# Optimization experiments

Hardware: AMD Instinct MI355X
Metric: run time of the kernel (lower is better)

Reference implementation:

```python
import jax, jax.numpy as jnp
import numpy as np

# Geometry: 256x256 image, 16x16 superpixel grid (cell=16), K=256, C=20 features, B=4.
B, H, W, C, KG = 4, 256, 256, 20, 16
K = KG * KG
CELL = H // KG
BIG_DIST = 1e4  # additive distance for non-neighbor superpixels


def setup_inputs() -> dict:
    key = jax.random.key(0)
    kf, = jax.random.split(key, 1)
    # initial hard pixel->superpixel grid assignment (get_spixel_init)
    gy = jnp.arange(H) // CELL
    gx = jnp.arange(W) // CELL
    spixel_init = (gy[:, None] * KG + gx[None, :]).reshape(-1).astype(jnp.int32)  # [N]
    # 9-neighborhood validity mask (compute_neighbor_spix_idx)
    ky = jnp.arange(K) // KG
    kx = jnp.arange(K) % KG
    pgy = spixel_init // KG
    pgx = spixel_init % KG
    valid = ((jnp.abs(pgy[:, None] - ky[None, :]) <= 1)
             & (jnp.abs(pgx[:, None] - kx[None, :]) <= 1)).astype(jnp.float32)  # [N, K]
    adjust = (1.0 - valid) * BIG_DIST  # [N, K]
    features = jax.random.normal(kf, (B, H * W, C), dtype=jnp.float32)  # CNN output, flattened
    return {
        "features": features,
        "valid_spixel": valid,
        "adjust_dist": adjust,
        "spixel_init": spixel_init,
        "iter_EM": 10,
    }


def _e_step(mean, features, valid_spixel, adjust_dist):
    # squared distances via ||f||^2 - 2 f.m + ||m||^2 (bmm form)
    feat_sq = jnp.sum(features * features, axis=-1)        # [B, N]
    mean_sq = jnp.sum(mean * mean, axis=-1)                # [B, K]
    dot = jnp.einsum('bnc,bkc->bnk', features, mean)       # [B, N, K]
    dist_sq = feat_sq[:, :, None] - 2.0 * dot + mean_sq[:, None, :]
    dist_sq = dist_sq * valid_spixel[None] + adjust_dist[None]
    # std = 1/sqrt(2) => 2*std^2 = 1, so softmax argument is -dist_sq
    return jax.nn.softmax(-dist_sq, axis=2)                # [B, N, K]


def _m_step(features, posteriors):
    # L1-normalize posteriors over the pixel axis (dim=1), then weighted mean
    col = jnp.maximum(jnp.sum(posteriors, axis=1, keepdims=True), 1e-12)
    post_norm = posteriors / col
    return jnp.einsum('bnk,bnc->bkc', post_norm, features)  # [B, K, C]


def reference(features, valid_spixel, adjust_dist, spixel_init, iter_EM):
    # compute_init_spixel_feat: mean of features within each initial superpixel (detached in torch)
    n = features.shape[1]
    sums = jax.vmap(lambda f: jax.ops.segment_sum(f, spixel_init, num_segments=K))(features)  # [B, K, C]
    counts = jax.ops.segment_sum(jnp.ones((n,), features.dtype), spixel_init, num_segments=K)  # [K]
    mean = jax.lax.stop_gradient(sums / jnp.maximum(counts, 1.0)[None, :, None])
    for _ in range(int(iter_EM) - 1):
        posteriors = _e_step(mean, features, valid_spixel, adjust_dist)
        mean = _m_step(features, posteriors)
    return _e_step(mean, features, valid_spixel, adjust_dist)
```

## Files before the change

### kernel.cpp

```cpp
#include <hip/hip_runtime.h>


#define NBATCH 4
#define WIMG   256
#define NC     20
#define NCS    21
#define NKG    16
#define NK     256
#define NPIX   65536
#define CELLSZ 16
#define LDST   260

__device__ __forceinline__ float dot4f(const float4 a, const float4 b) {
    return fmaf(a.x, b.x, fmaf(a.y, b.y, fmaf(a.z, b.z, a.w * b.w)));
}

__device__ __forceinline__ void load_feat(const float* __restrict__ feat, int b, int n, float f[NC]) {
    const float4* fp = (const float4*)(feat + ((size_t)b * NPIX + n) * NC);
    #pragma unroll
    for (int i = 0; i < 5; ++i) {
        float4 v = fp[i];
        f[4 * i + 0] = v.x; f[4 * i + 1] = v.y; f[4 * i + 2] = v.z; f[4 * i + 3] = v.w;
    }
}

__device__ __forceinline__ void e_step(const float* f, int b, int cy, int cx,
                                       const float* __restrict__ Sprev, float p[9]) {
    float a[9];
    float amax = -1e30f;
    #pragma unroll
    for (int dy = -1; dy <= 1; ++dy) {
        #pragma unroll
        for (int dx = -1; dx <= 1; ++dx) {
            int j = (dy + 1) * 3 + (dx + 1);
            int ky = cy + dy, kx = cx + dx;
            if (ky >= 0 && ky < NKG && kx >= 0 && kx < NKG) {
                const float* sp = Sprev + ((size_t)(b * NK + ky * NKG + kx)) * NCS;
                float dots = 0.f, ssq = 0.f;
                #pragma unroll
                for (int c = 0; c < NC; ++c) {
                    float sv = sp[c];
                    dots = fmaf(f[c], sv, dots);
                    ssq  = fmaf(sv, sv, ssq);
                }
                float col = fmaxf(sp[NC], 1e-12f);
                float r = 1.0f / col;
                a[j] = 2.0f * r * dots - (r * r) * ssq;
                amax = fmaxf(amax, a[j]);
            } else {
                a[j] = -1e30f;
            }
        }
    }
    float esum = 0.f;
    #pragma unroll
    for (int j = 0; j < 9; ++j) {
        float e = (a[j] > -1e29f) ? __expf(a[j] - amax) : 0.0f;
        p[j] = e;
        esum += e;
    }
    float inv = 1.0f / esum;
    #pragma unroll
    for (int j = 0; j < 9; ++j) p[j] *= inv;
}

__global__ __launch_bounds__(256, 4) void k_init(const float* __restrict__ feat,
                                                 float* __restrict__ S0,
                                                 float* __restrict__ S1) {
    __shared__ float fT[NC * LDST];
    int blk = blockIdx.x;
    int b = blk >> 8, k0 = blk & 255;
    int cy = k0 >> 4, cx = k0 & 15;
    int t = threadIdx.x;
    int ly = t >> 4, lx = t & 15;
    int n = (cy * CELLSZ + ly) * WIMG + cx * CELLSZ + lx;
    float f[NC];
    load_feat(feat, b, n, f);
    #pragma unroll
    for (int c = 0; c < NC; ++c) fT[c * LDST + t] = f[c];
    __syncthreads();
    if (t < NCS) {
        float s;
        if (t == NC) {
            s = 256.0f;
        } else {
            s = 0.f;
            const float4* row = (const float4*)&fT[t * LDST];
            #pragma unroll 4
            for (int i = 0; i < 64; ++i) { float4 v = row[i]; s += v.x + v.y + v.z + v.w; }
        }
        size_t off = ((size_t)(b * NK + k0)) * NCS + t;
        S0[off] = s;
        S1[off] = 0.0f;
    }
}

__global__ __launch_bounds__(256, 4) void k_em(const float* __restrict__ feat,
                                               const float* __restrict__ Sprev,
                                               float* __restrict__ Snext,
                                               float* __restrict__ Szero) {
    __shared__ float fT[NCS * LDST];
    __shared__ float pT[9 * LDST];
    __shared__ float part[21 * 8 * 9];
    int blk = blockIdx.x;
    int b = blk >> 8, k0 = blk & 255;
    int cy = k0 >> 4, cx = k0 & 15;
    int t = threadIdx.x;
    int ly = t >> 4, lx = t & 15;
    int n = (cy * CELLSZ + ly) * WIMG + cx * CELLSZ + lx;
    float f[NC];
    load_feat(feat, b, n, f);
    #pragma unroll
    for (int c = 0; c < NC; ++c) fT[c * LDST + t] = f[c];
    fT[NC * LDST + t] = 1.0f;
    float p[9];
    e_step(f, b, cy, cx, Sprev, p);
    #pragma unroll
    for (int j = 0; j < 9; ++j) pT[j * LDST + t] = p[j];
    __syncthreads();

    if (t < 168) {
        int tile = t >> 3, kid = t & 7;
        int j0 = (tile / 7) * 3, c0 = (tile % 7) * 3;
        float acc[3][3] = {};
        #pragma unroll
        for (int ch = 0; ch < 8; ++ch) {
            int nb = kid * 32 + (((ch + kid) & 7) << 2);
            float4 pv[3], fv[3];
            #pragma unroll
            for (int jj = 0; jj < 3; ++jj) pv[jj] = *(const float4*)&pT[(j0 + jj) * LDST + nb];
            #pragma unroll
            for (int cc = 0; cc < 3; ++cc) fv[cc] = *(const float4*)&fT[(c0 + cc) * LDST + nb];
            #pragma unroll
            for (int jj = 0; jj < 3; ++jj)
                #pragma unroll
                for (int cc = 0; cc < 3; ++cc)
                    acc[jj][cc] += dot4f(pv[jj], fv[cc]);
        }
        #pragma unroll
        for (int jj = 0; jj < 3; ++jj)
            #pragma unroll
            for (int cc = 0; cc < 3; ++cc)
                part[tile * 72 + kid * 9 + jj * 3 + cc] = acc[jj][cc];
    }
    __syncthreads();
    if (t < 189) {
        int j = t / 21, c = t % 21;
        int tile = (j / 3) * 7 + (c / 3);
        int elem = (j % 3) * 3 + (c % 3);
        float s = 0.f;
        #pragma unroll
        for (int kid = 0; kid < 8; ++kid) s += part[tile * 72 + kid * 9 + elem];
        int ky = cy + (j / 3) - 1, kx = cx + (j % 3) - 1;
        if (ky >= 0 && ky < NKG && kx >= 0 && kx < NKG)
            atomicAdd(&Snext[((size_t)(b * NK + ky * NKG + kx)) * NCS + c], s);
    }
    if (t < NCS) Szero[((size_t)(b * NK + k0)) * NCS + t] = 0.0f;
}

__global__ __launch_bounds__(256, 4) void k_final(const float* __restrict__ feat,
                                                  const float* __restrict__ Sprev,
                                                  float* __restrict__ out) {
    __shared__ float pT[9 * LDST];
    int blk = blockIdx.x;
    int b = blk >> 8, k0 = blk & 255;
    int cy = k0 >> 4, cx = k0 & 15;
    int t = threadIdx.x;
    int ly = t >> 4, lx = t & 15;
    int n = (cy * CELLSZ + ly) * WIMG + cx * CELLSZ + lx;
    float f[NC];
    load_feat(feat, b, n, f);
    float p[9];
    e_step(f, b, cy, cx, Sprev, p);
    #pragma unroll
    for (int j = 0; j < 9; ++j) pT[j * LDST + t] = p[j];
    __syncthreads();

    int wv = t >> 6, ln = t & 63;
    int j4[4];
    #pragma unroll
    for (int q = 0; q < 4; ++q) {
        int k = 4 * ln + q;
        int ky = k >> 4, kx = k & 15;
        int dy = ky - cy, dx = kx - cx;
        j4[q] = (dy >= -1 && dy <= 1 && dx >= -1 && dx <= 1) ? (dy + 1) * 3 + (dx + 1) : -1;
    }
    for (int i = 0; i < 64; ++i) {
        int pix = wv * 64 + i;
        int py = pix >> 4, px = pix & 15;
        int np = (cy * CELLSZ + py) * WIMG + cx * CELLSZ + px;
        float4 o;
        o.x = (j4[0] >= 0) ? pT[j4[0] * LDST + pix] : 0.0f;
        o.y = (j4[1] >= 0) ? pT[j4[1] * LDST + pix] : 0.0f;
        o.z = (j4[2] >= 0) ? pT[j4[2] * LDST + pix] : 0.0f;
        o.w = (j4[3] >= 0) ? pT[j4[3] * LDST + pix] : 0.0f;
        size_t rowoff = ((size_t)(b * NPIX + np)) * (size_t)NK;
        *(float4*)(out + rowoff + 4 * ln) = o;
    }
}

extern "C" void kernel_launch(void* const* d_in, const int* in_sizes, int n_in,
                              void* d_out, int out_size, void* d_ws, size_t ws_size,
                              hipStream_t stream) {
    (void)in_sizes; (void)n_in; (void)out_size; (void)ws_size;
    const float* feat = (const float*)d_in[0];
    float* out = (float*)d_out;
    const size_t SB = (size_t)NBATCH * NK * NCS;
    float* bufs[3] = { (float*)d_ws, (float*)d_ws + SB, (float*)d_ws + 2 * SB };

    dim3 grid(NBATCH * NK), block(256);
    k_init<<<grid, block, 0, stream>>>(feat, bufs[0], bufs[1]);
    for (int i = 1; i <= 9; ++i) {
        k_em<<<grid, block, 0, stream>>>(feat, bufs[(i - 1) % 3], bufs[i % 3], bufs[(i + 1) % 3]);
    }
    k_final<<<grid, block, 0, stream>>>(feat, bufs[0], out);
}
```

Baseline: 545.4 us.

## Fuse init, EM iterations and final step into one cooperative persistent kernel

Replaces the eleven separate kernel launches with a single cooperative kernel that keeps each block's pixel features in registers and shared memory across all EM iterations, separating iterations with grid-wide syncs. This removes launch gaps and repeated feature loads from global memory. It depends on all 1024 blocks being co-resident; if the cooperative launch fails it falls back to the original multi-kernel path. Grid syncs add their own latency per iteration.

New measurement: 1.810 ms. 3.32x slower.

```diff
diff --git a/kernel.cpp b/kernel.cpp
--- a/kernel.cpp
+++ b/kernel.cpp
@@ -1,4 +1,7 @@
 #include <hip/hip_runtime.h>
+#include <hip/hip_cooperative_groups.h>
+
+namespace cg = cooperative_groups;
 
 
 #define NBATCH 4
@@ -62,6 +65,128 @@
     float inv = 1.0f / esum;
     #pragma unroll
     for (int j = 0; j < 9; ++j) p[j] *= inv;
+}
+
+__global__ __launch_bounds__(256, 4) void k_ssn(const float* __restrict__ feat,
+                                                float* S0, float* S1, float* S2,
+                                                float* __restrict__ out) {
+    cg::grid_group gg = cg::this_grid();
+    __shared__ float fT[NCS * LDST];
+    __shared__ float pT[9 * LDST];
+    __shared__ float part[21 * 8 * 9];
+
+    float* bufs[3] = { S0, S1, S2 };
+    int blk = blockIdx.x;
+    int b = blk >> 8, k0 = blk & 255;
+    int cy = k0 >> 4, cx = k0 & 15;
+    int t = threadIdx.x;
+    int ly = t >> 4, lx = t & 15;
+    int n = (cy * CELLSZ + ly) * WIMG + cx * CELLSZ + lx;
+
+    float f[NC];
+    load_feat(feat, b, n, f);
+    #pragma unroll
+    for (int c = 0; c < NC; ++c) fT[c * LDST + t] = f[c];
+    fT[NC * LDST + t] = 1.0f;
+    __syncthreads();
+
+    if (t < NCS) {
+        float s;
+        if (t == NC) {
+            s = 256.0f;
+        } else {
+            s = 0.f;
+            const float4* row = (const float4*)&fT[t * LDST];
+            #pragma unroll 4
+            for (int i = 0; i < 64; ++i) { float4 v = row[i]; s += v.x + v.y + v.z + v.w; }
+        }
+        size_t off = ((size_t)(b * NK + k0)) * NCS + t;
+        S0[off] = s;
+        S1[off] = 0.0f;
+    }
+    gg.sync();
+
+    for (int it = 1; it <= 9; ++it) {
+        const float* __restrict__ Sprev = bufs[(it - 1) % 3];
+        float* Snext = bufs[it % 3];
+        float* Szero = bufs[(it + 1) % 3];
+
+        float p[9];
+        e_step(f, b, cy, cx, Sprev, p);
+        #pragma unroll
+        for (int j = 0; j < 9; ++j) pT[j * LDST + t] = p[j];
+        __syncthreads();
+
+        if (t < 168) {
+            int tile = t >> 3, kid = t & 7;
+            int j0 = (tile / 7) * 3, c0 = (tile % 7) * 3;
+            float acc[3][3] = {};
+            #pragma unroll
+            for (int ch = 0; ch < 8; ++ch) {
+                int nb = kid * 32 + (((ch + kid) & 7) << 2);
+                float4 pv[3], fv[3];
+                #pragma unroll
+                for (int jj = 0; jj < 3; ++jj) pv[jj] = *(const float4*)&pT[(j0 + jj) * LDST + nb];
+                #pragma unroll
+                for (int cc = 0; cc < 3; ++cc) fv[cc] = *(const float4*)&fT[(c0 + cc) * LDST + nb];
+                #pragma unroll
+                for (int jj = 0; jj < 3; ++jj)
+                    #pragma unroll
+                    for (int cc = 0; cc < 3; ++cc)
+                        acc[jj][cc] += dot4f(pv[jj], fv[cc]);
+            }
+            #pragma unroll
+            for (int jj = 0; jj < 3; ++jj)
+                #pragma unroll
+                for (int cc = 0; cc < 3; ++cc)
+                    part[tile * 72 + kid * 9 + jj * 3 + cc] = acc[jj][cc];
+        }
+        __syncthreads();
+        if (t < 189) {
+            int j = t / 21, c = t % 21;
+            int tile = (j / 3) * 7 + (c / 3);
+            int elem = (j % 3) * 3 + (c % 3);
+            float s = 0.f;
+            #pragma unroll
+            for (int kid = 0; kid < 8; ++kid) s += part[tile * 72 + kid * 9 + elem];
+            int ky = cy + (j / 3) - 1, kx = cx + (j % 3) - 1;
+            if (ky >= 0 && ky < NKG && kx >= 0 && kx < NKG)
+                atomicAdd(&Snext[((size_t)(b * NK + ky * NKG + kx)) * NCS + c], s);
+        }
+        if (t < NCS) Szero[((size_t)(b * NK + k0)) * NCS + t] = 0.0f;
+        gg.sync();
+    }
+
+    {
+        const float* __restrict__ Sprev = bufs[0];
+        float p[9];
+        e_step(f, b, cy, cx, Sprev, p);
+        #pragma unroll
+        for (int j = 0; j < 9; ++j) pT[j * LDST + t] = p[j];
+        __syncthreads();
+
+        int wv = t >> 6, ln = t & 63;
+        int j4[4];
+        #pragma unroll
+        for (int q = 0; q < 4; ++q) {
+            int k = 4 * ln + q;
+            int ky = k >> 4, kx = k & 15;
+            int dy = ky - cy, dx = kx - cx;
+            j4[q] = (dy >= -1 && dy <= 1 && dx >= -1 && dx <= 1) ? (dy + 1) * 3 + (dx + 1) : -1;
+        }
+        for (int i = 0; i < 64; ++i) {
+            int pix = wv * 64 + i;
+            int py = pix >> 4, px = pix & 15;
+            int np = (cy * CELLSZ + py) * WIMG + cx * CELLSZ + px;
+            float4 o;
+            o.x = (j4[0] >= 0) ? pT[j4[0] * LDST + pix] : 0.0f;
+            o.y = (j4[1] >= 0) ? pT[j4[1] * LDST + pix] : 0.0f;
+            o.z = (j4[2] >= 0) ? pT[j4[2] * LDST + pix] : 0.0f;
+            o.w = (j4[3] >= 0) ? pT[j4[3] * LDST + pix] : 0.0f;
+            size_t rowoff = ((size_t)(b * NPIX + np)) * (size_t)NK;
+            *(float4*)(out + rowoff + 4 * ln) = o;
+        }
+    }
 }
 
 __global__ __launch_bounds__(256, 4) void k_init(const float* __restrict__ feat,
@@ -118,7 +243,6 @@
     #pragma unroll
     for (int j = 0; j < 9; ++j) pT[j * LDST + t] = p[j];
     __syncthreads();
-
     if (t < 168) {
         int tile = t >> 3, kid = t & 7;
         int j0 = (tile / 7) * 3, c0 = (tile % 7) * 3;
@@ -175,7 +299,6 @@
     #pragma unroll
     for (int j = 0; j < 9; ++j) pT[j * LDST + t] = p[j];
     __syncthreads();
-
     int wv = t >> 6, ln = t & 63;
     int j4[4];
     #pragma unroll
@@ -206,12 +329,18 @@
     const float* feat = (const float*)d_in[0];
     float* out = (float*)d_out;
     const size_t SB = (size_t)NBATCH * NK * NCS;
-    float* bufs[3] = { (float*)d_ws, (float*)d_ws + SB, (float*)d_ws + 2 * SB };
+    float* s0 = (float*)d_ws;
+    float* s1 = (float*)d_ws + SB;
+    float* s2 = (float*)d_ws + 2 * SB;
 
     dim3 grid(NBATCH * NK), block(256);
-    k_init<<<grid, block, 0, stream>>>(feat, bufs[0], bufs[1]);
-    for (int i = 1; i <= 9; ++i) {
-        k_em<<<grid, block, 0, stream>>>(feat, bufs[(i - 1) % 3], bufs[i % 3], bufs[(i + 1) % 3]);
-    }
-    k_final<<<grid, block, 0, stream>>>(feat, bufs[0], out);
-}
+    void* args[] = { (void*)&feat, (void*)&s0, (void*)&s1, (void*)&s2, (void*)&out };
+    hipError_t err = hipLaunchCooperativeKernel((const void*)k_ssn, grid, block, args, 0, stream);
+    if (err != hipSuccess) {
+        float* bufs[3] = { s0, s1, s2 };
+        k_init<<<grid, block, 0, stream>>>(feat, bufs[0], bufs[1]);
+        for (int i = 1; i <= 9; ++i)
+            k_em<<<grid, block, 0, stream>>>(feat, bufs[(i - 1) % 3], bufs[i % 3], bufs[(i + 1) % 3]);
+        k_final<<<grid, block, 0, stream>>>(feat, bufs[0], out);
+    }
+}
```
